# Optimization experiments

Hardware: AMD Instinct MI355X
Metric: run time of the kernel (lower is better)

Reference implementation:

```python
import jax, jax.numpy as jnp
import numpy as np

EPS = 1e-5
TAU = 2.0
NUM_HEADS = 8
SCALE = 0.125

# Heaviside spike with sigmoid surrogate gradient (spikingjelly default, alpha=4)
@jax.custom_vjp
def spike_fn(x):
    return (x >= 0).astype(x.dtype)

def _spike_fwd(x):
    return spike_fn(x), x

def _spike_bwd(x, g):
    alpha = 4.0
    s = jax.nn.sigmoid(alpha * x)
    return (g * alpha * s * (1.0 - s),)

spike_fn.defvjp(_spike_fwd, _spike_bwd)

def lif(x, v_th):
    # MultiStepLIFNode: v += (x - v)/tau; spike = H(v - v_th); hard reset v=0 (detach_reset)
    def step(v, xt):
        v = v + (xt - v) / TAU
        s = spike_fn(v - v_th)
        v = v * (1.0 - jax.lax.stop_gradient(s))
        return v, s
    _, s = jax.lax.scan(step, jnp.zeros_like(x[0]), x)
    return s

def bn(y, g, b, m, rv):
    # BatchNorm1d in eval mode over channel dim C (last dim here, since torch code
    # transposes to (TB,C,N) before BN and back after)
    return (y - m) * (g * jax.lax.rsqrt(rv + EPS)) + b

def setup_inputs():
    key = jax.random.key(0)
    T, B, N, C = 4, 8, 512, 512
    ks = jax.random.split(key, 16)
    d = {"x": jax.random.normal(ks[0], (T, B, N, C), jnp.float32)}
    i = 1
    for name in ("q", "k", "v", "p"):
        d[f"w{name}"] = jax.random.normal(ks[i], (C, C), jnp.float32) * 0.02; i += 1
        d[f"b{name}"] = jnp.zeros((C,), jnp.float32)
        d[f"g{name}"] = jnp.ones((C,), jnp.float32)
        d[f"beta{name}"] = jnp.zeros((C,), jnp.float32)
        d[f"m{name}"] = jax.random.normal(ks[i], (C,), jnp.float32) * 0.1; i += 1
        d[f"rv{name}"] = jax.random.uniform(ks[i], (C,), jnp.float32, minval=0.5, maxval=1.5); i += 1
    return d

def reference(x, wq, bq, gq, betaq, mq, rvq,
              wk, bk, gk, betak, mk, rvk,
              wv, bv, gv, betav, mv, rvv,
              wp, bp, gp, betap, mp, rvp):
    T, B, N, C = x.shape
    H = NUM_HEADS
    D = C // H
    xf = x.reshape(T * B, N, C)

    def branch(w, b, g, be, m, rv):
        # Linear -> BN(eval) -> LIF -> split heads
        # (k/v paths in the torch code reshape to (T,B,C,N) between BN and LIF, but
        # since those are pure reshapes of the same flat buffer and LIF is elementwise
        # per timestep, the math is identical to the q path.)
        y = bn(jnp.einsum('bnc,oc->bno', xf, w) + b, g, be, m, rv).reshape(T, B, N, C)
        s = lif(y, 1.0)
        return s.reshape(T, B, N, H, D).transpose(0, 1, 3, 2, 4)  # (T,B,H,N,D)

    q = branch(wq, bq, gq, betaq, mq, rvq)
    k = branch(wk, bk, gk, betak, mk, rvk)
    v = branch(wv, bv, gv, betav, mv, rvv)

    attn = jnp.einsum('tbhnd,tbhmd->tbhnm', q, k) * SCALE  # no softmax
    o = jnp.einsum('tbhnm,tbhmd->tbhnd', attn, v)
    o = o.transpose(0, 1, 3, 2, 4).reshape(T, B, N, C)
    o = lif(o, 0.5)  # attn_lif, v_threshold=0.5

    y = bn(jnp.einsum('bnc,oc->bno', o.reshape(T * B, N, C), wp) + bp,
           gp, betap, mp, rvp).reshape(T, B, N, C)
    return lif(y, 1.0)  # proj_lif
```

## Files before the change

kernel.cpp:

```cpp
#include <hip/hip_runtime.h>
#include <hip/hip_bf16.h>

typedef _Float16 h8 __attribute__((ext_vector_type(8)));
typedef float f4 __attribute__((ext_vector_type(4)));

#define T_ 4
#define B_ 8
#define N_ 512
#define C_ 512
#define H_ 8
#define D_ 64
#define BNR 4096
#define EPSf 1e-5f
#define F16_MIN_NORM 6.1035156e-05f
#define INV4096 0.000244140625f

__global__ __launch_bounds__(256)
void split_pack_x(const float* __restrict__ in, _Float16* __restrict__ h1,
                  _Float16* __restrict__ h2)
{
    const int gid = blockIdx.x * 256 + threadIdx.x;
    const int lane = gid & 63;
    const int ks = (gid >> 6) & 15;
    const int t = (gid >> 10) & 3;
    const int rt = gid >> 12;
    const int row = rt * 16 + (lane & 15);
    const size_t src = ((size_t)t * BNR + row) * C_ + ks * 32 + (lane >> 4) * 8;
    const float4 x0 = *reinterpret_cast<const float4*>(in + src);
    const float4 x1 = *reinterpret_cast<const float4*>(in + src + 4);
    h8 a, b;
    #pragma unroll
    for (int j = 0; j < 8; ++j) {
        const float xv = (j < 4) ? (&x0.x)[j] : (&x1.x)[j - 4];
        const float hi = (fabsf(xv) >= F16_MIN_NORM) ? xv : 0.0f;
        const _Float16 h = (_Float16)hi;
        const float r = (xv - (float)h) * 4096.0f;
        a[j] = h; b[j] = (_Float16)r;
    }
    *reinterpret_cast<h8*>(h1 + (size_t)gid * 8) = a;
    *reinterpret_cast<h8*>(h2 + (size_t)gid * 8) = b;
}

__device__ __forceinline__
void pack_w_one(const float* __restrict__ W, _Float16* __restrict__ Wp1,
                _Float16* __restrict__ Wp2, int gid)
{
    const int lane = gid & 63;
    const int ni = (gid >> 6) & 3;
    const int ks = (gid >> 8) & 15;
    const int ct = gid >> 12;
    const int col = ct * 64 + ni * 16 + (lane & 15);
    const int k = ks * 32 + (lane >> 4) * 8;
    const float* src = W + (size_t)col * C_ + k;
    h8 a, b;
    #pragma unroll
    for (int j = 0; j < 8; ++j) {
        const float xv = src[j];
        const float hi = (fabsf(xv) >= F16_MIN_NORM) ? xv : 0.0f;
        const _Float16 h = (_Float16)hi;
        const float r = (xv - (float)h) * 4096.0f;
        a[j] = h; b[j] = (_Float16)r;
    }
    *reinterpret_cast<h8*>(Wp1 + (size_t)gid * 8) = a;
    *reinterpret_cast<h8*>(Wp2 + (size_t)gid * 8) = b;
}

__global__ __launch_bounds__(256)
void pack_w_all(const float* __restrict__ Wq, const float* __restrict__ Wk,
                const float* __restrict__ Wv, const float* __restrict__ Wp,
                _Float16* q1, _Float16* q2, _Float16* k1, _Float16* k2,
                _Float16* v1, _Float16* v2, _Float16* p1, _Float16* p2)
{
    const int g = blockIdx.x * 256 + threadIdx.x;
    const int br = g >> 15;
    const int gid = g & 32767;
    if (br == 0)      pack_w_one(Wq, q1, q2, gid);
    else if (br == 1) pack_w_one(Wk, k1, k2, gid);
    else if (br == 2) pack_w_one(Wv, v1, v2, gid);
    else              pack_w_one(Wp, p1, p2, gid);
}

__global__ __launch_bounds__(512, 4)
void gemm3_bn_lif(const _Float16* __restrict__ A1p, const _Float16* __restrict__ A2p,
                  const _Float16* __restrict__ Wq1, const _Float16* __restrict__ Wq2,
                  const _Float16* __restrict__ Wk1, const _Float16* __restrict__ Wk2,
                  const _Float16* __restrict__ Wv1, const _Float16* __restrict__ Wv2,
                  const float* __restrict__ biq, const float* __restrict__ gaq,
                  const float* __restrict__ beq, const float* __restrict__ meq,
                  const float* __restrict__ rvq,
                  const float* __restrict__ bik, const float* __restrict__ gak,
                  const float* __restrict__ bek, const float* __restrict__ mek,
                  const float* __restrict__ rvk,
                  const float* __restrict__ biv, const float* __restrict__ gav,
                  const float* __restrict__ bev, const float* __restrict__ mev,
                  const float* __restrict__ rvv,
                  _Float16* __restrict__ oq, _Float16* __restrict__ ok,
                  _Float16* __restrict__ ov)
{
    __shared__ __align__(16) char wsm[16384];
    const int br = blockIdx.y;
    const _Float16* W1 = (br == 0) ? Wq1 : (br == 1) ? Wk1 : Wv1;
    const _Float16* W2 = (br == 0) ? Wq2 : (br == 1) ? Wk2 : Wv2;
    const float* bias = (br == 0) ? biq : (br == 1) ? bik : biv;
    const float* gam  = (br == 0) ? gaq : (br == 1) ? gak : gav;
    const float* bet  = (br == 0) ? beq : (br == 1) ? bek : bev;
    const float* mea  = (br == 0) ? meq : (br == 1) ? mek : mev;
    const float* rva  = (br == 0) ? rvq : (br == 1) ? rvk : rvv;
    _Float16* out = (br == 0) ? oq : (br == 1) ? ok : ov;

    const int id = blockIdx.x;
    const int bt = (id & 7) * 8 + ((id >> 3) & 7);
    const int ct = id >> 6;
    const int tid = threadIdx.x;
    const int wave = tid >> 6, lane = tid & 63;
    const int tp = wave & 1, wr = wave >> 1;
    const int rt = bt * 4 + wr;
    const int row0 = bt * 64, col0 = ct * 64;
    const int lr = lane & 15, lk = lane >> 4;

    f4 accA[2][4], accB[2][4];
    #pragma unroll
    for (int ti = 0; ti < 2; ++ti)
        #pragma unroll
        for (int ni = 0; ni < 4; ++ni) { accA[ti][ni] = (f4)0.0f; accB[ti][ni] = (f4)0.0f; }

    const _Float16* aB1 = A1p + (size_t)rt * 32768 + lane * 8;
    const _Float16* aB2 = A2p + (size_t)rt * 32768 + lane * 8;
    const int s_ = wave >> 2, q_ = wave & 3;
    const _Float16* wsrc = (s_ ? W2 : W1) + (size_t)ct * 32768 + q_ * 512 + lane * 8;
    const int wdoff = s_ * 4096 + q_ * 1024;

    auto stageW = [&](int ks, int b) {
        __builtin_amdgcn_global_load_lds(
            (const __attribute__((address_space(1))) unsigned int*)(wsrc + ks * 2048),
            (__attribute__((address_space(3))) unsigned int*)(wsm + b * 8192 + wdoff),
            16, 0, 0);
    };

    stageW(0, 0);
    #pragma unroll 2
    for (int ks = 0; ks < 16; ++ks) {
        const int buf = ks & 1;
        __syncthreads();
        if (ks < 15) stageW(ks + 1, buf ^ 1);
        h8 a1[2], a2[2];
        #pragma unroll
        for (int ti = 0; ti < 2; ++ti) {
            const int t = tp * 2 + ti;
            a1[ti] = *reinterpret_cast<const h8*>(aB1 + (t * 16 + ks) * 512);
            a2[ti] = *reinterpret_cast<const h8*>(aB2 + (t * 16 + ks) * 512);
        }
        const char* wb = wsm + buf * 8192;
        #pragma unroll
        for (int ni = 0; ni < 4; ++ni) {
            const h8 wf1 = *reinterpret_cast<const h8*>(wb + ni * 1024 + lane * 16);
            const h8 wf2 = *reinterpret_cast<const h8*>(wb + 4096 + ni * 1024 + lane * 16);
            #pragma unroll
            for (int ti = 0; ti < 2; ++ti) {
                accA[ti][ni] = __builtin_amdgcn_mfma_f32_16x16x32_f16(a1[ti], wf1, accA[ti][ni], 0, 0, 0);
                accB[ti][ni] = __builtin_amdgcn_mfma_f32_16x16x32_f16(a1[ti], wf2, accB[ti][ni], 0, 0, 0);
                accB[ti][ni] = __builtin_amdgcn_mfma_f32_16x16x32_f16(a2[ti], wf1, accB[ti][ni], 0, 0, 0);
            }
        }
    }

    float* vst = (float*)wsm;
    float sc[4], bi[4], mn[4], be[4];
    #pragma unroll
    for (int ni = 0; ni < 4; ++ni) {
        const int c = col0 + ni * 16 + lr;
        sc[ni] = gam[c] * (1.0f / sqrtf(rva[c] + EPSf));
        bi[ni] = bias[c]; mn[ni] = mea[c]; be[ni] = bet[c];
    }
    __syncthreads();
    if (tp == 0) {
        #pragma unroll
        for (int ni = 0; ni < 4; ++ni)
            #pragma unroll
            for (int r = 0; r < 4; ++r) {
                const int rl = wr * 16 + lk * 4 + r;
                const int bn = row0 + rl;
                float vm = 0.0f;
                #pragma unroll
                for (int ti = 0; ti < 2; ++ti) {
                    const float res = accA[ti][ni][r] + INV4096 * accB[ti][ni][r];
                    const float y = ((res + bi[ni]) - mn[ni]) * sc[ni] + be[ni];
                    vm = vm + (y - vm) * 0.5f;
                    const float s = (vm >= 1.0f) ? 1.0f : 0.0f;
                    vm = (s != 0.0f) ? 0.0f : vm;
                    const int b = bn >> 9, n = bn & 511;
                    out[((((size_t)ti * B_ + b) * H_ + ct) * N_ + n) * D_ + ni * 16 + lr] =
                        (_Float16)s;
                }
                vst[rl * 64 + ni * 16 + lr] = vm;
            }
    }
    __syncthreads();
    if (tp == 1) {
        #pragma unroll
        for (int ni = 0; ni < 4; ++ni)
            #pragma unroll
            for (int r = 0; r < 4; ++r) {
                const int rl = wr * 16 + lk * 4 + r;
                const int bn = row0 + rl;
                float vm = vst[rl * 64 + ni * 16 + lr];
                #pragma unroll
                for (int ti = 0; ti < 2; ++ti) {
                    const float res = accA[ti][ni][r] + INV4096 * accB[ti][ni][r];
                    const float y = ((res + bi[ni]) - mn[ni]) * sc[ni] + be[ni];
                    vm = vm + (y - vm) * 0.5f;
                    const float s = (vm >= 1.0f) ? 1.0f : 0.0f;
                    vm = (s != 0.0f) ? 0.0f : vm;
                    const int b = bn >> 9, n = bn & 511;
                    out[((((size_t)(2 + ti) * B_ + b) * H_ + ct) * N_ + n) * D_ + ni * 16 + lr] =
                        (_Float16)s;
                }
            }
    }
}

__global__ __launch_bounds__(512, 4)
void gemm_p_bn_lif(const _Float16* __restrict__ A1p,
                   const _Float16* __restrict__ Wp1, const _Float16* __restrict__ Wp2,
                   const float* __restrict__ bias, const float* __restrict__ gam,
                   const float* __restrict__ bet, const float* __restrict__ mea,
                   const float* __restrict__ rva, float* __restrict__ out_plain)
{
    __shared__ __align__(16) char wsm[65536];
    const int id = blockIdx.x;
    const int bt = (id & 7) * 8 + ((id >> 3) & 7);
    const int ct = id >> 6;
    const int tid = threadIdx.x;
    const int wave = tid >> 6, lane = tid & 63;
    const int tp = wave & 1, wr = wave >> 1;
    const int rt = bt * 4 + wr;
    const int row0 = bt * 64, col0 = ct * 64;
    const int lr = lane & 15, lk = lane >> 4;

    f4 accA[2][4], accB[2][4];
    #pragma unroll
    for (int ti = 0; ti < 2; ++ti)
        #pragma unroll
        for (int ni = 0; ni < 4; ++ni) { accA[ti][ni] = (f4)0.0f; accB[ti][ni] = (f4)0.0f; }

    const _Float16* aB1 = A1p + (size_t)rt * 32768 + lane * 8;
    const int s_ = wave >> 2, q_ = wave & 3;
    const _Float16* wsrc = (s_ ? Wp2 : Wp1) + (size_t)ct * 32768 + q_ * 512 + lane * 8;
    const int wdoff = s_ * 4096 + q_ * 1024;

    auto stageChunk = [&](int c, int b) {
        #pragma unroll
        for (int ksl = 0; ksl < 4; ++ksl) {
            __builtin_amdgcn_global_load_lds(
                (const __attribute__((address_space(1))) unsigned int*)(wsrc + (c * 4 + ksl) * 2048),
                (__attribute__((address_space(3))) unsigned int*)(wsm + b * 32768 + ksl * 8192 + wdoff),
                16, 0, 0);
        }
    };

    stageChunk(0, 0);
    #pragma unroll
    for (int c = 0; c < 4; ++c) {
        const int buf = c & 1;
        __syncthreads();
        if (c < 3) stageChunk(c + 1, buf ^ 1);
        #pragma unroll
        for (int ksl = 0; ksl < 4; ++ksl) {
            const int ks = c * 4 + ksl;
            h8 a1[2];
            #pragma unroll
            for (int ti = 0; ti < 2; ++ti) {
                const int t = tp * 2 + ti;
                a1[ti] = *reinterpret_cast<const h8*>(aB1 + (t * 16 + ks) * 512);
            }
            const char* wb = wsm + buf * 32768 + ksl * 8192;
            #pragma unroll
            for (int ni = 0; ni < 4; ++ni) {
                const h8 wf1 = *reinterpret_cast<const h8*>(wb + ni * 1024 + lane * 16);
                const h8 wf2 = *reinterpret_cast<const h8*>(wb + 4096 + ni * 1024 + lane * 16);
                #pragma unroll
                for (int ti = 0; ti < 2; ++ti) {
                    accA[ti][ni] = __builtin_amdgcn_mfma_f32_16x16x32_f16(a1[ti], wf1, accA[ti][ni], 0, 0, 0);
                    accB[ti][ni] = __builtin_amdgcn_mfma_f32_16x16x32_f16(a1[ti], wf2, accB[ti][ni], 0, 0, 0);
                }
            }
        }
    }

    float* vst = (float*)wsm;
    float sc[4], bi[4], mn[4], be[4];
    #pragma unroll
    for (int ni = 0; ni < 4; ++ni) {
        const int c = col0 + ni * 16 + lr;
        sc[ni] = gam[c] * (1.0f / sqrtf(rva[c] + EPSf));
        bi[ni] = bias[c]; mn[ni] = mea[c]; be[ni] = bet[c];
    }
    __syncthreads();
    if (tp == 0) {
        #pragma unroll
        for (int ni = 0; ni < 4; ++ni)
            #pragma unroll
            for (int r = 0; r < 4; ++r) {
                const int rl = wr * 16 + lk * 4 + r;
                const int bn = row0 + rl;
                float vm = 0.0f;
                #pragma unroll
                for (int ti = 0; ti < 2; ++ti) {
                    const float res = accA[ti][ni][r] + INV4096 * accB[ti][ni][r];
                    const float y = ((res + bi[ni]) - mn[ni]) * sc[ni] + be[ni];
                    vm = vm + (y - vm) * 0.5f;
                    const float s = (vm >= 1.0f) ? 1.0f : 0.0f;
                    vm = (s != 0.0f) ? 0.0f : vm;
                    out_plain[((size_t)ti * BNR + bn) * C_ + col0 + ni * 16 + lr] = s;
                }
                vst[rl * 64 + ni * 16 + lr] = vm;
            }
    }
    __syncthreads();
    if (tp == 1) {
        #pragma unroll
        for (int ni = 0; ni < 4; ++ni)
            #pragma unroll
            for (int r = 0; r < 4; ++r) {
                const int rl = wr * 16 + lk * 4 + r;
                const int bn = row0 + rl;
                float vm = vst[rl * 64 + ni * 16 + lr];
                #pragma unroll
                for (int ti = 0; ti < 2; ++ti) {
                    const float res = accA[ti][ni][r] + INV4096 * accB[ti][ni][r];
                    const float y = ((res + bi[ni]) - mn[ni]) * sc[ni] + be[ni];
                    vm = vm + (y - vm) * 0.5f;
                    const float s = (vm >= 1.0f) ? 1.0f : 0.0f;
                    vm = (s != 0.0f) ? 0.0f : vm;
                    out_plain[((size_t)(2 + ti) * BNR + bn) * C_ + col0 + ni * 16 + lr] = s;
                }
            }
    }
}

__global__ __launch_bounds__(256)
void ktv_kernel(const _Float16* __restrict__ sk, const _Float16* __restrict__ sv,
                _Float16* __restrict__ kvT)
{
    __shared__ _Float16 kl[64][64];
    __shared__ _Float16 vl[64][64];
    const int tbh = blockIdx.x;
    const int tid = threadIdx.x;
    const int tx = tid & 15, ty = tid >> 4;
    const size_t base = (size_t)tbh * N_ * D_;
    float acc[4][4] = {};
    for (int n0 = 0; n0 < N_; n0 += 64) {
        __syncthreads();
        #pragma unroll
        for (int p = 0; p < 2; ++p) {
            const int idx = tid + p * 256;
            const int r = idx >> 3, c8 = (idx & 7) * 8;
            *reinterpret_cast<float4*>(&kl[r][c8]) =
                *reinterpret_cast<const float4*>(&sk[base + (size_t)(n0 + r) * D_ + c8]);
            *reinterpret_cast<float4*>(&vl[r][c8]) =
                *reinterpret_cast<const float4*>(&sv[base + (size_t)(n0 + r) * D_ + c8]);
        }
        __syncthreads();
        for (int nn = 0; nn < 64; ++nn) {
            float a[4], b[4];
            #pragma unroll
            for (int i = 0; i < 4; ++i) a[i] = (float)kl[nn][ty * 4 + i];
            #pragma unroll
            for (int j = 0; j < 4; ++j) b[j] = (float)vl[nn][tx * 4 + j];
            #pragma unroll
            for (int i = 0; i < 4; ++i)
                #pragma unroll
                for (int j = 0; j < 4; ++j)
                    acc[i][j] = fmaf(a[i], b[j], acc[i][j]);
        }
    }
    _Float16* out = kvT + (size_t)tbh * 4096;
    #pragma unroll
    for (int i = 0; i < 4; ++i)
        #pragma unroll
        for (int j = 0; j < 4; ++j)
            out[(tx * 4 + j) * 64 + ty * 4 + i] = (_Float16)acc[i][j];
}

__global__ __launch_bounds__(256)
void qkv_mfma_lif(const _Float16* __restrict__ sq, const _Float16* __restrict__ kvT,
                  _Float16* __restrict__ osp)
{
    __shared__ __align__(16) char ot[8192];
    const int nt = blockIdx.x, b = blockIdx.y, h = blockIdx.z;
    const int tid = threadIdx.x;
    const int wv = tid >> 6, lane = tid & 63;
    const int lr = lane & 15, lk = lane >> 4;
    const int n0 = nt * 64;

    f4 vst[4];
    #pragma unroll
    for (int ni = 0; ni < 4; ++ni) vst[ni] = (f4)0.0f;

    for (int t = 0; t < T_; ++t) {
        const int tbh = (t * B_ + b) * H_ + h;
        const _Float16* qb = sq + ((size_t)tbh * N_ + n0 + wv * 16 + lr) * D_;
        const h8 a0 = *reinterpret_cast<const h8*>(qb + lk * 8);
        const h8 a1 = *reinterpret_cast<const h8*>(qb + 32 + lk * 8);
        const _Float16* kb = kvT + (size_t)tbh * 4096 + lr * 64 + lk * 8;
        f4 acc[4];
        #pragma unroll
        for (int ni = 0; ni < 4; ++ni) {
            const _Float16* kbn = kb + ni * 1024;
            const h8 b0 = *reinterpret_cast<const h8*>(kbn);
            const h8 b1 = *reinterpret_cast<const h8*>(kbn + 32);
            f4 a = (f4)0.0f;
            a = __builtin_amdgcn_mfma_f32_16x16x32_f16(a0, b0, a, 0, 0, 0);
            a = __builtin_amdgcn_mfma_f32_16x16x32_f16(a1, b1, a, 0, 0, 0);
            acc[ni] = a;
        }
        #pragma unroll
        for (int ni = 0; ni < 4; ++ni)
            #pragma unroll
            for (int r = 0; r < 4; ++r) {
                const float y = 0.125f * acc[ni][r];
                float vv = vst[ni][r];
                vv = vv + (y - vv) * 0.5f;
                const float s = (vv >= 0.5f) ? 1.0f : 0.0f;
                vst[ni][r] = (s != 0.0f) ? 0.0f : vv;
                const int row = wv * 16 + lk * 4 + r;
                const int colb = (ni * 16 + lr) * 2;
                *(_Float16*)(ot + row * 128 + (colb ^ ((row & 7) << 4))) = (_Float16)s;
            }
        const int rt = b * 32 + nt * 4 + wv;
        #pragma unroll
        for (int ks1 = 0; ks1 < 2; ++ks1) {
            const int row = wv * 16 + lr;
            const int colb = ks1 * 64 + lk * 16;
            const h8 vvv = *reinterpret_cast<const h8*>(ot + row * 128 + (colb ^ ((row & 7) << 4)));
            *reinterpret_cast<h8*>(osp +
                ((((size_t)rt * 4 + t) * 16 + h * 2 + ks1) * 64 + lane) * 8) = vvv;
        }
    }
}

extern "C" void kernel_launch(void* const* d_in, const int* in_sizes, int n_in,
                              void* d_out, int out_size, void* d_ws, size_t ws_size,
                              hipStream_t stream)
{
    const float* x = (const float*)d_in[0];
    const float *W[4], *bia[4], *gam[4], *bet[4], *mea[4], *rva[4];
    for (int br = 0; br < 4; ++br) {
        W[br]   = (const float*)d_in[1 + 6 * br + 0];
        bia[br] = (const float*)d_in[1 + 6 * br + 1];
        gam[br] = (const float*)d_in[1 + 6 * br + 2];
        bet[br] = (const float*)d_in[1 + 6 * br + 3];
        mea[br] = (const float*)d_in[1 + 6 * br + 4];
        rva[br] = (const float*)d_in[1 + 6 * br + 5];
    }
    char* ws = (char*)d_ws;
    _Float16* x1 = (_Float16*)(ws + 0);
    _Float16* x2 = (_Float16*)(ws + 16777216);
    _Float16* sq = (_Float16*)(ws + 33554432);
    _Float16* sk = (_Float16*)(ws + 50331648);
    _Float16* sv = (_Float16*)(ws + 67108864);
    _Float16* w1[4], *w2[4];
    for (int br = 0; br < 4; ++br) {
        w1[br] = (_Float16*)(ws + 83886080 + (size_t)br * 1048576);
        w2[br] = (_Float16*)(ws + 83886080 + (size_t)br * 1048576 + 524288);
    }
    _Float16* kvT = (_Float16*)(ws + 16777216);
    _Float16* osp = (_Float16*)(ws + 0);

    dim3 blk(256);
    split_pack_x<<<dim3(4096), blk, 0, stream>>>(x, x1, x2);
    pack_w_all<<<dim3(512), blk, 0, stream>>>(W[0], W[1], W[2], W[3],
        w1[0], w2[0], w1[1], w2[1], w1[2], w2[2], w1[3], w2[3]);

    gemm3_bn_lif<<<dim3(512, 3), dim3(512), 0, stream>>>(x1, x2,
        w1[0], w2[0], w1[1], w2[1], w1[2], w2[2],
        bia[0], gam[0], bet[0], mea[0], rva[0],
        bia[1], gam[1], bet[1], mea[1], rva[1],
        bia[2], gam[2], bet[2], mea[2], rva[2],
        sq, sk, sv);

    ktv_kernel<<<dim3(T_ * B_ * H_), blk, 0, stream>>>(sk, sv, kvT);
    qkv_mfma_lif<<<dim3(N_ / 64, B_, H_), blk, 0, stream>>>(sq, kvT, osp);

    gemm_p_bn_lif<<<dim3(512), dim3(512), 0, stream>>>(osp, w1[3], w2[3],
        bia[3], gam[3], bet[3], mea[3], rva[3], (float*)d_out);
}
```

Baseline: 167.4 us.

## Fuse Q/K/V branches into one block to share activation loads

Each block now computes all three projection branches (Q, K, V) for a 32-row by 64-column tile, so the A fragments loaded from global memory are reused across the three weight matrices instead of being fetched three times by separate grid.y blocks. The wave layout changes so each wave pair handles one timestep, and the LIF recurrence is serialized across timesteps through shared-memory membrane state with barriers between steps. This triples accumulator registers and LDS use (48KB), which may lower occupancy, and adds more barriers in the epilogue.

```diff
diff --git a/kernel.cpp b/kernel.cpp
--- a/kernel.cpp
+++ b/kernel.cpp
@@ -97,44 +97,49 @@
                   _Float16* __restrict__ oq, _Float16* __restrict__ ok,
                   _Float16* __restrict__ ov)
 {
-    __shared__ __align__(16) char wsm[16384];
-    const int br = blockIdx.y;
-    const _Float16* W1 = (br == 0) ? Wq1 : (br == 1) ? Wk1 : Wv1;
-    const _Float16* W2 = (br == 0) ? Wq2 : (br == 1) ? Wk2 : Wv2;
-    const float* bias = (br == 0) ? biq : (br == 1) ? bik : biv;
-    const float* gam  = (br == 0) ? gaq : (br == 1) ? gak : gav;
-    const float* bet  = (br == 0) ? beq : (br == 1) ? bek : bev;
-    const float* mea  = (br == 0) ? meq : (br == 1) ? mek : mev;
-    const float* rva  = (br == 0) ? rvq : (br == 1) ? rvk : rvv;
-    _Float16* out = (br == 0) ? oq : (br == 1) ? ok : ov;
+    __shared__ __align__(16) char smem[49152];
+    const _Float16* W1a[3] = {Wq1, Wk1, Wv1};
+    const _Float16* W2a[3] = {Wq2, Wk2, Wv2};
+    const float* biasa[3] = {biq, bik, biv};
+    const float* gama[3]  = {gaq, gak, gav};
+    const float* betaa[3] = {beq, bek, bev};
+    const float* meaa[3]  = {meq, mek, mev};
+    const float* rvaa[3]  = {rvq, rvk, rvv};
+    _Float16* outa[3] = {oq, ok, ov};
 
     const int id = blockIdx.x;
-    const int bt = (id & 7) * 8 + ((id >> 3) & 7);
-    const int ct = id >> 6;
+    const int bt = (id & 7) * 16 + ((id >> 3) & 15);
+    const int ct = id >> 7;
     const int tid = threadIdx.x;
     const int wave = tid >> 6, lane = tid & 63;
-    const int tp = wave & 1, wr = wave >> 1;
-    const int rt = bt * 4 + wr;
-    const int row0 = bt * 64, col0 = ct * 64;
+    const int tp = wave >> 1, wr = wave & 1;
+    const int rt = bt * 2 + wr;
+    const int row0 = bt * 32, col0 = ct * 64;
     const int lr = lane & 15, lk = lane >> 4;
 
-    f4 accA[2][4], accB[2][4];
-    #pragma unroll
-    for (int ti = 0; ti < 2; ++ti)
-        #pragma unroll
-        for (int ni = 0; ni < 4; ++ni) { accA[ti][ni] = (f4)0.0f; accB[ti][ni] = (f4)0.0f; }
+    f4 accA[3][4], accB[3][4];
+    #pragma unroll
+    for (int br = 0; br < 3; ++br)
+        #pragma unroll
+        for (int ni = 0; ni < 4; ++ni) { accA[br][ni] = (f4)0.0f; accB[br][ni] = (f4)0.0f; }
 
     const _Float16* aB1 = A1p + (size_t)rt * 32768 + lane * 8;
     const _Float16* aB2 = A2p + (size_t)rt * 32768 + lane * 8;
     const int s_ = wave >> 2, q_ = wave & 3;
-    const _Float16* wsrc = (s_ ? W2 : W1) + (size_t)ct * 32768 + q_ * 512 + lane * 8;
+    const _Float16* wsrc[3];
+    #pragma unroll
+    for (int i = 0; i < 3; ++i)
+        wsrc[i] = (s_ ? W2a[i] : W1a[i]) + (size_t)ct * 32768 + q_ * 512 + lane * 8;
     const int wdoff = s_ * 4096 + q_ * 1024;
 
     auto stageW = [&](int ks, int b) {
-        __builtin_amdgcn_global_load_lds(
-            (const __attribute__((address_space(1))) unsigned int*)(wsrc + ks * 2048),
-            (__attribute__((address_space(3))) unsigned int*)(wsm + b * 8192 + wdoff),
-            16, 0, 0);
+        #pragma unroll
+        for (int i = 0; i < 3; ++i) {
+            __builtin_amdgcn_global_load_lds(
+                (const __attribute__((address_space(1))) unsigned int*)(wsrc[i] + ks * 2048),
+                (__attribute__((address_space(3))) unsigned int*)(smem + b * 24576 + i * 8192 + wdoff),
+                16, 0, 0);
+        }
     };
 
     stageW(0, 0);
@@ -143,79 +148,55 @@
         const int buf = ks & 1;
         __syncthreads();
         if (ks < 15) stageW(ks + 1, buf ^ 1);
-        h8 a1[2], a2[2];
-        #pragma unroll
-        for (int ti = 0; ti < 2; ++ti) {
-            const int t = tp * 2 + ti;
-            a1[ti] = *reinterpret_cast<const h8*>(aB1 + (t * 16 + ks) * 512);
-            a2[ti] = *reinterpret_cast<const h8*>(aB2 + (t * 16 + ks) * 512);
-        }
-        const char* wb = wsm + buf * 8192;
-        #pragma unroll
-        for (int ni = 0; ni < 4; ++ni) {
-            const h8 wf1 = *reinterpret_cast<const h8*>(wb + ni * 1024 + lane * 16);
-            const h8 wf2 = *reinterpret_cast<const h8*>(wb + 4096 + ni * 1024 + lane * 16);
-            #pragma unroll
-            for (int ti = 0; ti < 2; ++ti) {
-                accA[ti][ni] = __builtin_amdgcn_mfma_f32_16x16x32_f16(a1[ti], wf1, accA[ti][ni], 0, 0, 0);
-                accB[ti][ni] = __builtin_amdgcn_mfma_f32_16x16x32_f16(a1[ti], wf2, accB[ti][ni], 0, 0, 0);
-                accB[ti][ni] = __builtin_amdgcn_mfma_f32_16x16x32_f16(a2[ti], wf1, accB[ti][ni], 0, 0, 0);
-            }
-        }
-    }
-
-    float* vst = (float*)wsm;
-    float sc[4], bi[4], mn[4], be[4];
-    #pragma unroll
-    for (int ni = 0; ni < 4; ++ni) {
-        const int c = col0 + ni * 16 + lr;
-        sc[ni] = gam[c] * (1.0f / sqrtf(rva[c] + EPSf));
-        bi[ni] = bias[c]; mn[ni] = mea[c]; be[ni] = bet[c];
-    }
+        const h8 a1 = *reinterpret_cast<const h8*>(aB1 + (tp * 16 + ks) * 512);
+        const h8 a2 = *reinterpret_cast<const h8*>(aB2 + (tp * 16 + ks) * 512);
+        const char* wb = smem + buf * 24576;
+        #pragma unroll
+        for (int br = 0; br < 3; ++br)
+            #pragma unroll
+            for (int ni = 0; ni < 4; ++ni) {
+                const h8 wf1 = *reinterpret_cast<const h8*>(wb + br * 8192 + ni * 1024 + lane * 16);
+                const h8 wf2 = *reinterpret_cast<const h8*>(wb + br * 8192 + 4096 + ni * 1024 + lane * 16);
+                accA[br][ni] = __builtin_amdgcn_mfma_f32_16x16x32_f16(a1, wf1, accA[br][ni], 0, 0, 0);
+                accB[br][ni] = __builtin_amdgcn_mfma_f32_16x16x32_f16(a1, wf2, accB[br][ni], 0, 0, 0);
+                accB[br][ni] = __builtin_amdgcn_mfma_f32_16x16x32_f16(a2, wf1, accB[br][ni], 0, 0, 0);
+            }
+    }
+
+    float* vst = (float*)smem;
     __syncthreads();
-    if (tp == 0) {
-        #pragma unroll
-        for (int ni = 0; ni < 4; ++ni)
-            #pragma unroll
-            for (int r = 0; r < 4; ++r) {
-                const int rl = wr * 16 + lk * 4 + r;
-                const int bn = row0 + rl;
-                float vm = 0.0f;
-                #pragma unroll
-                for (int ti = 0; ti < 2; ++ti) {
-                    const float res = accA[ti][ni][r] + INV4096 * accB[ti][ni][r];
-                    const float y = ((res + bi[ni]) - mn[ni]) * sc[ni] + be[ni];
-                    vm = vm + (y - vm) * 0.5f;
-                    const float s = (vm >= 1.0f) ? 1.0f : 0.0f;
-                    vm = (s != 0.0f) ? 0.0f : vm;
-                    const int b = bn >> 9, n = bn & 511;
-                    out[((((size_t)ti * B_ + b) * H_ + ct) * N_ + n) * D_ + ni * 16 + lr] =
-                        (_Float16)s;
+    #pragma unroll
+    for (int ts = 0; ts < 4; ++ts) {
+        if (tp == ts) {
+            #pragma unroll
+            for (int br = 0; br < 3; ++br) {
+                float sc[4], bi[4], mn[4], be[4];
+                #pragma unroll
+                for (int ni = 0; ni < 4; ++ni) {
+                    const int c = col0 + ni * 16 + lr;
+                    sc[ni] = gama[br][c] * (1.0f / sqrtf(rvaa[br][c] + EPSf));
+                    bi[ni] = biasa[br][c]; mn[ni] = meaa[br][c]; be[ni] = betaa[br][c];
                 }
-                vst[rl * 64 + ni * 16 + lr] = vm;
-            }
-    }
-    __syncthreads();
-    if (tp == 1) {
-        #pragma unroll
-        for (int ni = 0; ni < 4; ++ni)
-            #pragma unroll
-            for (int r = 0; r < 4; ++r) {
-                const int rl = wr * 16 + lk * 4 + r;
-                const int bn = row0 + rl;
-                float vm = vst[rl * 64 + ni * 16 + lr];
-                #pragma unroll
-                for (int ti = 0; ti < 2; ++ti) {
-                    const float res = accA[ti][ni][r] + INV4096 * accB[ti][ni][r];
-                    const float y = ((res + bi[ni]) - mn[ni]) * sc[ni] + be[ni];
-                    vm = vm + (y - vm) * 0.5f;
-                    const float s = (vm >= 1.0f) ? 1.0f : 0.0f;
-                    vm = (s != 0.0f) ? 0.0f : vm;
-                    const int b = bn >> 9, n = bn & 511;
-                    out[((((size_t)(2 + ti) * B_ + b) * H_ + ct) * N_ + n) * D_ + ni * 16 + lr] =
-                        (_Float16)s;
-                }
-            }
+                #pragma unroll
+                for (int ni = 0; ni < 4; ++ni)
+                    #pragma unroll
+                    for (int r = 0; r < 4; ++r) {
+                        const int rl = wr * 16 + lk * 4 + r;
+                        const int bn = row0 + rl;
+                        float vm = (ts == 0) ? 0.0f : vst[(br * 32 + rl) * 64 + ni * 16 + lr];
+                        const float res = accA[br][ni][r] + INV4096 * accB[br][ni][r];
+                        const float y = ((res + bi[ni]) - mn[ni]) * sc[ni] + be[ni];
+                        vm = vm + (y - vm) * 0.5f;
+                        const float s = (vm >= 1.0f) ? 1.0f : 0.0f;
+                        vm = (s != 0.0f) ? 0.0f : vm;
+                        const int b = bn >> 9, n = bn & 511;
+                        outa[br][((((size_t)ts * B_ + b) * H_ + ct) * N_ + n) * D_ + ni * 16 + lr] =
+                            (_Float16)s;
+                        if (ts < 3) vst[(br * 32 + rl) * 64 + ni * 16 + lr] = vm;
+                    }
+            }
+        }
+        if (ts < 3) __syncthreads();
     }
 }
 
@@ -472,7 +453,7 @@
     pack_w_all<<<dim3(512), blk, 0, stream>>>(W[0], W[1], W[2], W[3],
         w1[0], w2[0], w1[1], w2[1], w1[2], w2[2], w1[3], w2[3]);
 
-    gemm3_bn_lif<<<dim3(512, 3), dim3(512), 0, stream>>>(x1, x2,
+    gemm3_bn_lif<<<dim3(1024), dim3(512), 0, stream>>>(x1, x2,
         w1[0], w2[0], w1[1], w2[1], w1[2], w2[2],
         bia[0], gam[0], bet[0], mea[0], rva[0],
         bia[1], gam[1], bet[1], mea[1], rva[1],
```

New measurement: 320.3 us. 91.3% more time.
